# Kernel tuning notes

Hardware: AMD Instinct MI355X
Metric: run time of the kernel (lower is better)

## Reference

```python
import jax, jax.numpy as jnp
import numpy as np

NUM_FEATURES = 20480
NUM_ACCUMULATORS = 128


def setup_inputs() -> dict:
    key = jax.random.key(0)
    k1, k2, k3, k4, k5, k6 = jax.random.split(key, 6)
    B = 4096
    white = jax.random.uniform(k1, (B, NUM_FEATURES), dtype=jnp.float32)
    black = jax.random.uniform(k2, (B, NUM_FEATURES), dtype=jnp.float32)
    # learned params (torch nn.Linear stores weight as [out, in])
    w_psqt = jax.random.normal(k3, (2, NUM_FEATURES), dtype=jnp.float32) * 0.01
    w_acc = jax.random.normal(k4, (NUM_ACCUMULATORS, NUM_FEATURES), dtype=jnp.float32) * 0.01
    b_acc = jax.random.normal(k5, (NUM_ACCUMULATORS,), dtype=jnp.float32) * 0.01
    w_layer = jax.random.normal(k6, (2, NUM_ACCUMULATORS), dtype=jnp.float32) * 0.1
    return {"white": white, "black": black, "w_psqt": w_psqt,
            "w_acc": w_acc, "b_acc": b_acc, "w_layer": w_layer}


def reference(white, black, w_psqt, w_acc, b_acc, w_layer):
    # psqt: Linear(NUM_FEATURES -> 2, no bias)
    psqt = jnp.einsum('bf,of->bo', white, w_psqt) - jnp.einsum('bf,of->bo', black, w_psqt)
    # accumulator: Linear(NUM_FEATURES -> 128) + CReLU clamp(0, 1)
    white_acc = jnp.clip(jnp.einsum('bf,af->ba', white, w_acc) + b_acc, 0.0, 1.0)
    black_acc = jnp.clip(jnp.einsum('bf,af->ba', black, w_acc) + b_acc, 0.0, 1.0)
    # output layer: Linear(128 -> 2, no bias)
    positional = jnp.einsum('ba,oa->bo', white_acc, w_layer) - jnp.einsum('ba,oa->bo', black_acc, w_layer)
    return psqt + positional
```

## Files before the change

kernel.cpp:

```cpp
#include <hip/hip_runtime.h>
#include <hip/hip_bf16.h>
#include <stdint.h>

typedef __attribute__((ext_vector_type(4))) float          f32x4;
typedef __attribute__((ext_vector_type(8))) short          short8;
typedef __attribute__((ext_vector_type(4))) unsigned short u16x4;

#define F            20480
#define NROWS        4096
#define NPAD         144
#define BK           64
#define CHUNK_BYTES  (NPAD * BK * 2)
#define TOTAL_CHUNKS (F / BK)
#define MB           128

static __device__ __forceinline__ unsigned short f2bf(float f) {
    unsigned u = __builtin_bit_cast(unsigned, f);
    unsigned r = (u + 0x7FFFu + ((u >> 16) & 1u)) >> 16;
    return (unsigned short)r;
}

__global__ __launch_bounds__(256) void prep_b(const float* __restrict__ w_acc,
                                              const float* __restrict__ w_psqt,
                                              unsigned short* __restrict__ Bp) {
    int gid = blockIdx.x * 256 + threadIdx.x;
    int p8    = gid * 8;
    int chunk = p8 / CHUNK_BYTES;
    int win   = p8 % CHUNK_BYTES;
    int n     = win >> 7;
    int sb    = win & 127;
    int kbyte = sb ^ ((n & 7) << 4);
    int k0    = chunk * 64 + (kbyte >> 1);
    f32x4 v = {0.f, 0.f, 0.f, 0.f};
    if (n < 128)      v = *(const f32x4*)(w_acc  + (size_t)n * F + k0);
    else if (n < 130) v = *(const f32x4*)(w_psqt + (size_t)(n - 128) * F + k0);
    u16x4 pk;
    pk[0] = f2bf(v[0]); pk[1] = f2bf(v[1]); pk[2] = f2bf(v[2]); pk[3] = f2bf(v[3]);
    *(u16x4*)((char*)Bp + p8) = pk;
}

__global__ __launch_bounds__(256, 2) void gemm_main(
    const float* __restrict__ white, const float* __restrict__ black,
    const unsigned short* __restrict__ Bp, float* __restrict__ partial,
    int chunks_per_ks)
{
    __shared__ alignas(16) unsigned short Blds[2][CHUNK_BYTES / 2];

    const int tid  = threadIdx.x;
    const int wave = tid >> 6;
    const int lane = tid & 63;
    const int g    = lane >> 4;
    const int r16  = lane & 15;

    const int rg   = blockIdx.x;
    const int row0 = rg * MB;
    const float* Aside = (row0 < NROWS) ? white : black;
    const int arow0 = row0 & (NROWS - 1);

    const int chunk0 = blockIdx.y * chunks_per_ks;
    const int nch    = chunks_per_ks;

    const float* aRow0 = Aside + (size_t)(arow0 + wave * 32 + r16) * F + g * 8;
    const float* aRow1 = aRow0 + (size_t)16 * F;

    f32x4 apf[2][2][2];
    f32x4 acc[2][9];
    const f32x4 zero = {0.f, 0.f, 0.f, 0.f};
    #pragma unroll
    for (int m = 0; m < 2; ++m)
        #pragma unroll
        for (int n = 0; n < 9; ++n) acc[m][n] = zero;

    auto stageB = [&](int buf, int chunk) {
        const char* src = (const char*)Bp + (size_t)chunk * CHUNK_BYTES + lane * 16;
        char* dst = (char*)(&Blds[buf][0]);
        #pragma unroll
        for (int line = 0; line < 5; ++line) {
            int li = wave + line * 4;
            if (li < 18)
                __builtin_amdgcn_global_load_lds(
                    (const __attribute__((address_space(1))) void*)(src + li * 1024),
                    (__attribute__((address_space(3))) void*)(dst + li * 1024),
                    16, 0, 0);
        }
    };

    auto loadA = [&](int kbase) {
        const float* p0 = aRow0 + kbase;
        const float* p1 = aRow1 + kbase;
        apf[0][0][0] = *(const f32x4*)(p0);
        apf[0][0][1] = *(const f32x4*)(p0 + 4);
        apf[0][1][0] = *(const f32x4*)(p0 + 32);
        apf[0][1][1] = *(const f32x4*)(p0 + 36);
        apf[1][0][0] = *(const f32x4*)(p1);
        apf[1][0][1] = *(const f32x4*)(p1 + 4);
        apf[1][1][0] = *(const f32x4*)(p1 + 32);
        apf[1][1][1] = *(const f32x4*)(p1 + 36);
    };

    stageB(0, chunk0);
    loadA(chunk0 * BK);

    for (int t = 0; t < nch; ++t) {
        __syncthreads();

        short8 afr[2][2];
        #pragma unroll
        for (int m = 0; m < 2; ++m)
            #pragma unroll
            for (int kk = 0; kk < 2; ++kk) {
                short8 r;
                #pragma unroll
                for (int j = 0; j < 4; ++j) {
                    r[j]     = (short)f2bf(apf[m][kk][0][j]);
                    r[j + 4] = (short)f2bf(apf[m][kk][1][j]);
                }
                afr[m][kk] = r;
            }

        if (t + 1 < nch) {
            stageB((t + 1) & 1, chunk0 + t + 1);
            loadA((chunk0 + t + 1) * BK);
        }

        const char* bb = (const char*)(&Blds[t & 1][0]);
        #pragma unroll
        for (int kk = 0; kk < 2; ++kk) {
            #pragma unroll
            for (int n = 0; n < 9; ++n) {
                const int nn  = n * 16 + r16;
                const int off = nn * 128 + ((kk * 64 + g * 16) ^ ((nn & 7) << 4));
                short8 bf = *(const short8*)(bb + off);
                acc[0][n] = __builtin_amdgcn_mfma_f32_16x16x32_bf16(afr[0][kk], bf, acc[0][n], 0, 0, 0);
                acc[1][n] = __builtin_amdgcn_mfma_f32_16x16x32_bf16(afr[1][kk], bf, acc[1][n], 0, 0, 0);
            }
        }
    }

    float* prow = partial + ((size_t)blockIdx.y * 8192 + row0 + wave * 32 + g * 4) * NPAD;
    #pragma unroll
    for (int m = 0; m < 2; ++m)
        #pragma unroll
        for (int n = 0; n < 9; ++n)
            #pragma unroll
            for (int j = 0; j < 4; ++j)
                prow[(m * 16 + j) * NPAD + n * 16 + r16] = acc[m][n][j];
}

__global__ __launch_bounds__(256) void epilogue(
    const float* __restrict__ partial, const float* __restrict__ b_acc,
    const float* __restrict__ w_layer, float* __restrict__ out, int KS)
{
    const int wave = threadIdx.x >> 6, lane = threadIdx.x & 63;
    const int b = blockIdx.x * 4 + wave;
    float sw0 = 0, sw1 = 0, sb0 = 0, sb1 = 0, q0 = 0, q1 = 0;
    for (int ks = 0; ks < KS; ++ks) {
        const float* Pw = partial + ((size_t)ks * 8192 + b) * NPAD;
        const float* Pb = partial + ((size_t)ks * 8192 + NROWS + b) * NPAD;
        sw0 += Pw[lane];      sw1 += Pw[lane + 64];
        sb0 += Pb[lane];      sb1 += Pb[lane + 64];
        q0  += Pw[128] - Pb[128];
        q1  += Pw[129] - Pb[129];
    }
    float wa0 = fminf(fmaxf(sw0 + b_acc[lane], 0.f), 1.f);
    float wa1 = fminf(fmaxf(sw1 + b_acc[lane + 64], 0.f), 1.f);
    float ba0 = fminf(fmaxf(sb0 + b_acc[lane], 0.f), 1.f);
    float ba1 = fminf(fmaxf(sb1 + b_acc[lane + 64], 0.f), 1.f);
    float d0 = wa0 - ba0, d1 = wa1 - ba1;
    float p0 = w_layer[lane] * d0       + w_layer[lane + 64] * d1;
    float p1 = w_layer[128 + lane] * d0 + w_layer[192 + lane] * d1;
    #pragma unroll
    for (int off = 32; off >= 1; off >>= 1) {
        p0 += __shfl_xor(p0, off, 64);
        p1 += __shfl_xor(p1, off, 64);
    }
    if (lane == 0) {
        out[b * 2 + 0] = q0 + p0;
        out[b * 2 + 1] = q1 + p1;
    }
}

extern "C" void kernel_launch(void* const* d_in, const int* in_sizes, int n_in,
                              void* d_out, int out_size, void* d_ws, size_t ws_size,
                              hipStream_t stream)
{
    const float* white   = (const float*)d_in[0];
    const float* black   = (const float*)d_in[1];
    const float* w_psqt  = (const float*)d_in[2];
    const float* w_acc   = (const float*)d_in[3];
    const float* b_acc   = (const float*)d_in[4];
    const float* w_layer = (const float*)d_in[5];
    float* out = (float*)d_out;

    const size_t bbytes = (size_t)TOTAL_CHUNKS * CHUNK_BYTES;
    unsigned short* Bp = (unsigned short*)d_ws;
    float* partial = (float*)((char*)d_ws + bbytes);

    const size_t per_ks = (size_t)8192 * NPAD * 4;
    int KS = 1;
    const int cands[5] = {8, 5, 4, 2, 1};
    for (int i = 0; i < 5; ++i)
        if (bbytes + (size_t)cands[i] * per_ks <= ws_size) { KS = cands[i]; break; }
    int chunks_per_ks = TOTAL_CHUNKS / KS;

    prep_b   <<<dim3(2880),     dim3(256), 0, stream>>>(w_acc, w_psqt, Bp);
    gemm_main<<<dim3(64, KS),   dim3(256), 0, stream>>>(white, black, Bp, partial, chunks_per_ks);
    epilogue <<<dim3(1024),     dim3(256), 0, stream>>>(partial, b_acc, w_layer, out, KS);
}
```

Before: 167.8 us.

## Load B fragments directly from global memory, dropping LDS staging and block sync

The GEMM kernel no longer stages the packed weight chunk in shared memory through a double buffer with __syncthreads. Each wave now reads its bf16 B fragments straight from global memory, relying on L2/L1 since all waves share the small weight matrix. Work is assigned per wave, so the four waves of a block are independent and handle different row groups or K-splits. The XOR swizzle in the weight packing is removed because LDS bank conflicts no longer apply. The trade is more global and L1 traffic and less latency hiding for B loads, in exchange for no barriers and no LDS.

```diff
diff --git a/kernel.cpp b/kernel.cpp
--- a/kernel.cpp
+++ b/kernel.cpp
@@ -12,7 +12,6 @@
 #define BK           64
 #define CHUNK_BYTES  (NPAD * BK * 2)
 #define TOTAL_CHUNKS (F / BK)
-#define MB           128
 
 static __device__ __forceinline__ unsigned short f2bf(float f) {
     unsigned u = __builtin_bit_cast(unsigned, f);
@@ -29,8 +28,7 @@
     int win   = p8 % CHUNK_BYTES;
     int n     = win >> 7;
     int sb    = win & 127;
-    int kbyte = sb ^ ((n & 7) << 4);
-    int k0    = chunk * 64 + (kbyte >> 1);
+    int k0    = chunk * 64 + (sb >> 1);
     f32x4 v = {0.f, 0.f, 0.f, 0.f};
     if (n < 128)      v = *(const f32x4*)(w_acc  + (size_t)n * F + k0);
     else if (n < 130) v = *(const f32x4*)(w_psqt + (size_t)(n - 128) * F + k0);
@@ -44,24 +42,26 @@
     const unsigned short* __restrict__ Bp, float* __restrict__ partial,
     int chunks_per_ks)
 {
-    __shared__ alignas(16) unsigned short Blds[2][CHUNK_BYTES / 2];
-
     const int tid  = threadIdx.x;
     const int wave = tid >> 6;
     const int lane = tid & 63;
     const int g    = lane >> 4;
     const int r16  = lane & 15;
 
-    const int rg   = blockIdx.x;
-    const int row0 = rg * MB;
-    const float* Aside = (row0 < NROWS) ? white : black;
-    const int arow0 = row0 & (NROWS - 1);
+    const int wid = blockIdx.x * 4 + wave;
+    const int rg  = wid & 255;
+    const int ks  = wid >> 8;
 
-    const int chunk0 = blockIdx.y * chunks_per_ks;
+    const int grow0 = rg * 32;
+    const float* Aside = (grow0 < NROWS) ? white : black;
+    const int arow0 = grow0 & (NROWS - 1);
+
+    const int chunk0 = ks * chunks_per_ks;
     const int nch    = chunks_per_ks;
 
-    const float* aRow0 = Aside + (size_t)(arow0 + wave * 32 + r16) * F + g * 8;
+    const float* aRow0 = Aside + (size_t)(arow0 + r16) * F + g * 8;
     const float* aRow1 = aRow0 + (size_t)16 * F;
+    const char* bBase = (const char*)Bp + r16 * 128 + g * 16;
 
     f32x4 apf[2][2][2];
     f32x4 acc[2][9];
@@ -70,20 +70,6 @@
     for (int m = 0; m < 2; ++m)
         #pragma unroll
         for (int n = 0; n < 9; ++n) acc[m][n] = zero;
-
-    auto stageB = [&](int buf, int chunk) {
-        const char* src = (const char*)Bp + (size_t)chunk * CHUNK_BYTES + lane * 16;
-        char* dst = (char*)(&Blds[buf][0]);
-        #pragma unroll
-        for (int line = 0; line < 5; ++line) {
-            int li = wave + line * 4;
-            if (li < 18)
-                __builtin_amdgcn_global_load_lds(
-                    (const __attribute__((address_space(1))) void*)(src + li * 1024),
-                    (__attribute__((address_space(3))) void*)(dst + li * 1024),
-                    16, 0, 0);
-        }
-    };
 
     auto loadA = [&](int kbase) {
         const float* p0 = aRow0 + kbase;
@@ -98,11 +84,16 @@
         apf[1][1][1] = *(const f32x4*)(p1 + 36);
     };
 
-    stageB(0, chunk0);
     loadA(chunk0 * BK);
 
     for (int t = 0; t < nch; ++t) {
-        __syncthreads();
+        const char* bc = bBase + (size_t)(chunk0 + t) * CHUNK_BYTES;
+        short8 bfr[2][9];
+        #pragma unroll
+        for (int kk = 0; kk < 2; ++kk)
+            #pragma unroll
+            for (int n = 0; n < 9; ++n)
+                bfr[kk][n] = *(const short8*)(bc + n * 2048 + kk * 64);
 
         short8 afr[2][2];
         #pragma unroll
@@ -118,26 +109,18 @@
                 afr[m][kk] = r;
             }
 
-        if (t + 1 < nch) {
-            stageB((t + 1) & 1, chunk0 + t + 1);
-            loadA((chunk0 + t + 1) * BK);
-        }
+        if (t + 1 < nch) loadA((chunk0 + t + 1) * BK);
 
-        const char* bb = (const char*)(&Blds[t & 1][0]);
         #pragma unroll
-        for (int kk = 0; kk < 2; ++kk) {
+        for (int kk = 0; kk < 2; ++kk)
             #pragma unroll
             for (int n = 0; n < 9; ++n) {
-                const int nn  = n * 16 + r16;
-                const int off = nn * 128 + ((kk * 64 + g * 16) ^ ((nn & 7) << 4));
-                short8 bf = *(const short8*)(bb + off);
-                acc[0][n] = __builtin_amdgcn_mfma_f32_16x16x32_bf16(afr[0][kk], bf, acc[0][n], 0, 0, 0);
-                acc[1][n] = __builtin_amdgcn_mfma_f32_16x16x32_bf16(afr[1][kk], bf, acc[1][n], 0, 0, 0);
+                acc[0][n] = __builtin_amdgcn_mfma_f32_16x16x32_bf16(afr[0][kk], bfr[kk][n], acc[0][n], 0, 0, 0);
+                acc[1][n] = __builtin_amdgcn_mfma_f32_16x16x32_bf16(afr[1][kk], bfr[kk][n], acc[1][n], 0, 0, 0);
             }
-        }
     }
 
-    float* prow = partial + ((size_t)blockIdx.y * 8192 + row0 + wave * 32 + g * 4) * NPAD;
+    float* prow = partial + ((size_t)ks * 8192 + grow0 + g * 4) * NPAD;
     #pragma unroll
     for (int m = 0; m < 2; ++m)
         #pragma unroll
@@ -202,8 +185,9 @@
     for (int i = 0; i < 5; ++i)
         if (bbytes + (size_t)cands[i] * per_ks <= ws_size) { KS = cands[i]; break; }
     int chunks_per_ks = TOTAL_CHUNKS / KS;
+    int n_waves = 256 * KS;
 
-    prep_b   <<<dim3(2880),     dim3(256), 0, stream>>>(w_acc, w_psqt, Bp);
-    gemm_main<<<dim3(64, KS),   dim3(256), 0, stream>>>(white, black, Bp, partial, chunks_per_ks);
-    epilogue <<<dim3(1024),     dim3(256), 0, stream>>>(partial, b_acc, w_layer, out, KS);
+    prep_b   <<<dim3(2880),        dim3(256), 0, stream>>>(w_acc, w_psqt, Bp);
+    gemm_main<<<dim3(n_waves / 4), dim3(256), 0, stream>>>(white, black, Bp, partial, chunks_per_ks);
+    epilogue <<<dim3(1024),        dim3(256), 0, stream>>>(partial, b_acc, w_layer, out, KS);
 }
```

New measurement: 273.3 us. 62.9% more time.
